# Kernel optimization log

Measured on AMD Instinct MI355X. Metric: run time of the kernel, lower is better.

The kernel has to match this reference:

```python
import jax, jax.numpy as jnp
import numpy as np

D = 1024
H = 16
HD = D // H

def setup_inputs() -> dict:
    key = jax.random.key(0)
    ks = jax.random.split(key, 6)
    tokens = jax.random.normal(ks[0], (2, 2048, D), dtype=jnp.float32)
    # LayerNorm params
    ln_gamma = jnp.ones((D,), dtype=jnp.float32)
    ln_beta = jnp.zeros((D,), dtype=jnp.float32)
    # qkv Linear (no bias): torch Linear weight is [3D, D]; store as [D, 3D] for x @ W
    w_qkv = jax.random.normal(ks[1], (D, 3 * D), dtype=jnp.float32) / np.sqrt(D)
    # output projection with bias
    w_proj = jax.random.normal(ks[2], (D, D), dtype=jnp.float32) / np.sqrt(D)
    b_proj = jax.random.normal(ks[3], (D,), dtype=jnp.float32) * 0.01
    return {"tokens": tokens, "ln_gamma": ln_gamma, "ln_beta": ln_beta,
            "w_qkv": w_qkv, "w_proj": w_proj, "b_proj": b_proj}

def reference(tokens, ln_gamma, ln_beta, w_qkv, w_proj, b_proj):
    B, S, _ = tokens.shape
    res = tokens
    # LayerNorm (eps=1e-5, torch default)
    mu = jnp.mean(tokens, axis=-1, keepdims=True)
    var = jnp.var(tokens, axis=-1, keepdims=True)
    x = (tokens - mu) * jax.lax.rsqrt(var + 1e-5) * ln_gamma + ln_beta
    # QKV projection -> [B, S, 3, H, HD] -> q,k,v each [B, H, S, HD]
    qkv = (x @ w_qkv).reshape(B, S, 3, H, HD)
    qkv = jnp.transpose(qkv, (2, 0, 3, 1, 4))
    q, k, v = qkv[0], qkv[1], qkv[2]
    scale = HD ** -0.5
    scores = jnp.einsum('bhsd,bhtd->bhst', q, k) * scale  # [B,H,S,S]
    attn = jax.nn.softmax(scores, axis=-1)
    dots = jnp.einsum('bhst,bhtd->bhsd', attn, v)          # [B,H,S,HD]
    dots = jnp.transpose(dots, (0, 2, 1, 3)).reshape(B, S, D)
    out = dots @ w_proj + b_proj
    return out + res
```

## Files before the change

### kernel.cpp

```cpp
#include <hip/hip_runtime.h>

typedef __bf16 bf16x8 __attribute__((ext_vector_type(8)));
typedef __bf16 bf16x4 __attribute__((ext_vector_type(4)));
typedef float f32x4 __attribute__((ext_vector_type(4)));
typedef unsigned short us8 __attribute__((ext_vector_type(8)));

__device__ __forceinline__ unsigned short f2bf(float f) {
  unsigned int u = __builtin_bit_cast(unsigned int, f);
  u += 0x7FFFu + ((u >> 16) & 1u);
  return (unsigned short)(u >> 16);
}
__device__ __forceinline__ float bf2f(unsigned short s) {
  return __builtin_bit_cast(float, (unsigned int)s << 16);
}

__device__ __forceinline__ void load_lds16(const void* g, void* l) {
  __builtin_amdgcn_global_load_lds(
      (const __attribute__((address_space(1))) unsigned int*)g,
      (__attribute__((address_space(3))) unsigned int*)l, 16, 0, 0);
}

#define MFMA16(a, b, c) __builtin_amdgcn_mfma_f32_16x16x32_bf16(a, b, c, 0, 0, 0)
#define EXP2(x) __builtin_amdgcn_exp2f(x)

constexpr int Dm = 1024, Ss = 2048;

__global__ __launch_bounds__(256) void prep_kernel(
    const float* __restrict__ x, const float* __restrict__ gamma,
    const float* __restrict__ beta, unsigned short* __restrict__ xbf,
    const float* __restrict__ wqkv, unsigned short* __restrict__ wqkvT,
    const float* __restrict__ wproj, unsigned short* __restrict__ wprojT) {
  __shared__ float tile[32][33];
  const int t = threadIdx.x;
  if (blockIdx.x < 4096) {
    const int row = blockIdx.x;
    const float4 v = reinterpret_cast<const float4*>(x + (size_t)row * Dm)[t];
    float s = v.x + v.y + v.z + v.w;
    float ss = v.x * v.x + v.y * v.y + v.z * v.z + v.w * v.w;
#pragma unroll
    for (int off = 1; off < 64; off <<= 1) {
      s += __shfl_xor(s, off);
      ss += __shfl_xor(ss, off);
    }
    float* sb = &tile[0][0];
    const int lane = t & 63, wid = t >> 6;
    if (lane == 0) { sb[wid] = s; sb[4 + wid] = ss; }
    __syncthreads();
    s = sb[0] + sb[1] + sb[2] + sb[3];
    ss = sb[4] + sb[5] + sb[6] + sb[7];
    const float mu = s * (1.0f / Dm);
    const float var = ss * (1.0f / Dm) - mu * mu;
    const float rs = rsqrtf(var + 1e-5f);
    const float4 g = reinterpret_cast<const float4*>(gamma)[t];
    const float4 bt = reinterpret_cast<const float4*>(beta)[t];
    ushort4 pack;
    pack.x = f2bf((v.x - mu) * rs * g.x + bt.x);
    pack.y = f2bf((v.y - mu) * rs * g.y + bt.y);
    pack.z = f2bf((v.z - mu) * rs * g.z + bt.z);
    pack.w = f2bf((v.w - mu) * rs * g.w + bt.w);
    reinterpret_cast<ushort4*>(xbf + (size_t)row * Dm)[t] = pack;
  } else {
    const float* in;
    unsigned short* out;
    int N, bxi, byi;
    const int id0 = blockIdx.x - 4096;
    if (id0 < 3072) {
      in = wqkv; out = wqkvT; N = 3072;
      bxi = id0 % 96; byi = id0 / 96;
    } else {
      in = wproj; out = wprojT; N = 1024;
      const int id = id0 - 3072;
      bxi = id % 32; byi = id / 32;
    }
    const int tx = t & 31, ty = t >> 5;
    const int n0 = bxi * 32, k0 = byi * 32;
#pragma unroll
    for (int i = 0; i < 4; i++)
      tile[ty + i * 8][tx] = in[(size_t)(k0 + ty + i * 8) * N + n0 + tx];
    __syncthreads();
#pragma unroll
    for (int i = 0; i < 4; i++)
      out[(size_t)(n0 + ty + i * 8) * 1024 + k0 + tx] = f2bf(tile[tx][ty + i * 8]);
  }
}

__global__ __launch_bounds__(512) void gemm256_kernel(
    const unsigned short* __restrict__ A, const unsigned short* __restrict__ Bt,
    unsigned short* __restrict__ Cbf, unsigned short* __restrict__ vt) {
  extern __shared__ char lds[];
  const int tid = threadIdx.x;
  const int lane = tid & 63, wid = tid >> 6;
  const int l15 = lane & 15, lg = lane >> 4;
  const int wr = wid >> 2, wc = wid & 3;
  const int lb = (blockIdx.x & 7) * 24 + (blockIdx.x >> 3);
  const int bx = lb % 12, by = lb / 12;
  const int bm = by * 256, bn = bx * 256;
  const int sswz = ((lane & 3) * 16) ^ (((lane >> 3) & 3) << 4);
  const char* Asrc = (const char*)A + (size_t)(bm + wid * 32 + (lane >> 2)) * 2048 + sswz;
  const char* Bsrc = (const char*)Bt + (size_t)(bn + wid * 32 + (lane >> 2)) * 2048 + sswz;
  const int rdsz = ((lg * 16) ^ (((l15 >> 1) & 3) << 4));

#define STG_A(kk_, bufT, tile_)                                                 \
  if ((tile_) < 16) {                                                           \
    _Pragma("unroll") for (int c = 0; c < 2; c++)                               \
      load_lds16(Asrc + (size_t)(c * 16) * 2048 + (tile_) * 128 + (kk_) * 64,   \
                 lds + ((bufT) * 2 + (kk_)) * 16384 + wid * 2048 + c * 1024);   \
  }
#define STG_B(kk_, bufT, tile_)                                                 \
  if ((tile_) < 16) {                                                           \
    _Pragma("unroll") for (int c = 0; c < 2; c++)                               \
      load_lds16(Bsrc + (size_t)(c * 16) * 2048 + (tile_) * 128 + (kk_) * 64,   \
                 lds + 65536 + ((bufT) * 2 + (kk_)) * 16384 + wid * 2048 +      \
                     c * 1024);                                                 \
  }
#define DS_A(buf_, kk_)                                                         \
  _Pragma("unroll") for (int mi = 0; mi < 8; mi++) {                            \
    const int r = wr * 128 + mi * 16 + l15;                                     \
    af[mi] = *(const bf16x8*)(lds + ((buf_) * 2 + (kk_)) * 16384 + r * 64 + rdsz); \
  }
#define DS_B(buf_, kk_, nh_)                                                    \
  _Pragma("unroll") for (int nj = 0; nj < 2; nj++) {                            \
    const int r = wc * 64 + (nh_) * 32 + nj * 16 + l15;                         \
    bfr[nj] = *(const bf16x8*)(lds + 65536 + ((buf_) * 2 + (kk_)) * 16384 +     \
                               r * 64 + rdsz);                                  \
  }
#define MM(nh_)                                                                 \
  __builtin_amdgcn_s_setprio(1);                                                \
  _Pragma("unroll") for (int mi = 0; mi < 8; mi++)                              \
      _Pragma("unroll") for (int nj = 0; nj < 2; nj++)                          \
          acc[mi][(nh_) * 2 + nj] = MFMA16(af[mi], bfr[nj], acc[mi][(nh_) * 2 + nj]); \
  __builtin_amdgcn_s_setprio(0);
#define GBAR __builtin_amdgcn_s_barrier()
#define LGKM0 asm volatile("s_waitcnt lgkmcnt(0)" ::: "memory")

  f32x4 acc[8][4] = {};

  STG_A(0, 0, 0); STG_B(0, 0, 0); STG_A(1, 0, 0); STG_B(1, 0, 0);
  STG_A(0, 1, 1); STG_B(0, 1, 1); STG_A(1, 1, 1);
  asm volatile("s_waitcnt vmcnt(6)" ::: "memory");
  GBAR;

  for (int i = 0; i < 8; ++i) {
    const int t2 = 2 * i + 2, t3 = 2 * i + 3;
    const bool last = (i == 7);
    bf16x8 af[8], bfr[2];
    DS_A(0, 0); DS_B(0, 0, 0); STG_B(1, 1, 2 * i + 1);
    GBAR; LGKM0; MM(0); GBAR;
    DS_B(0, 0, 1); STG_A(0, 0, t2);
    GBAR; LGKM0; MM(1); GBAR;
    DS_A(0, 1); DS_B(0, 1, 0); STG_B(0, 0, t2);
    GBAR; LGKM0; MM(0); GBAR;
    DS_B(0, 1, 1); STG_A(1, 0, t2);
    GBAR; LGKM0; MM(1);
    if (last) asm volatile("s_waitcnt vmcnt(0)" ::: "memory");
    else      asm volatile("s_waitcnt vmcnt(6)" ::: "memory");
    GBAR;
    DS_A(1, 0); DS_B(1, 0, 0); STG_B(1, 0, t2);
    GBAR; LGKM0; MM(0); GBAR;
    DS_B(1, 0, 1); STG_A(0, 1, t3);
    GBAR; LGKM0; MM(1); GBAR;
    DS_A(1, 1); DS_B(1, 1, 0); STG_B(0, 1, t3);
    GBAR; LGKM0; MM(0); GBAR;
    DS_B(1, 1, 1); STG_A(1, 1, t3);
    GBAR; LGKM0; MM(1);
    if (last) asm volatile("s_waitcnt vmcnt(0)" ::: "memory");
    else      asm volatile("s_waitcnt vmcnt(6)" ::: "memory");
    GBAR;
  }

#pragma unroll
  for (int mi = 0; mi < 8; mi++)
#pragma unroll
    for (int nj = 0; nj < 4; nj++) {
      const int m = bm + wr * 128 + mi * 16 + lg * 4;
      const int n = bn + wc * 64 + nj * 16 + l15;
      if (n < 2048) {
        const float sc = (n < 1024) ? 0.180336880f : 1.0f;
#pragma unroll
        for (int r = 0; r < 4; r++)
          Cbf[(size_t)(m + r) * 3072 + n] = f2bf(acc[mi][nj][r] * sc);
      } else {
        const int h = (n - 2048) >> 6, hd = (n - 2048) & 63;
        const int bq = m >> 11, s = m & 2047;
        bf16x4 o;
#pragma unroll
        for (int r = 0; r < 4; r++) o[r] = (__bf16)acc[mi][nj][r];
        *(bf16x4*)(vt + ((size_t)((bq << 4) + h) * 64 + hd) * 2048 + s) = o;
      }
    }
#undef STG_A
#undef STG_B
#undef DS_A
#undef DS_B
#undef MM
#undef GBAR
#undef LGKM0
}

template <int EPI, int BN>
__global__ __launch_bounds__(256) void gemm_kernel(
    const unsigned short* __restrict__ A, const unsigned short* __restrict__ Bt,
    int N, int K, int nbx, unsigned short* __restrict__ Cbf,
    unsigned short* __restrict__ vt, float* __restrict__ Cf,
    const float* __restrict__ bias, const float* __restrict__ resid) {
  __shared__ unsigned short Al[128 * 64];
  __shared__ unsigned short Bl[BN * 64];
  constexpr int NJ = BN / 32;
  const int tid = threadIdx.x;
  const int lane = tid & 63, wid = tid >> 6;
  const int l15 = lane & 15, lg = lane >> 4;
  const int wm = wid >> 1, wn = wid & 1;
  const int cpx = gridDim.x >> 3;
  const int lb = (blockIdx.x & 7) * cpx + (blockIdx.x >> 3);
  const int bx = lb % nbx, by = lb / nbx;
  const int bm = by * 128, bn = bx * BN;
  const int r8 = lane >> 3;
  const int swz = ((lane & 7) * 16) ^ (r8 << 4);
  const char* Ab = (const char*)A;
  const char* Bb = (const char*)Bt;
  f32x4 acc[4][NJ] = {};
  for (int k0 = 0; k0 < K; k0 += 64) {
    __syncthreads();
#pragma unroll
    for (int p = 0; p < 4; p++) {
      const int row = p * 32 + wid * 8 + r8;
      load_lds16(Ab + ((size_t)(bm + row) * K + k0) * 2 + swz,
                 (char*)Al + p * 4096 + wid * 1024);
    }
#pragma unroll
    for (int p = 0; p < BN / 32; p++) {
      const int row = p * 32 + wid * 8 + r8;
      load_lds16(Bb + ((size_t)(bn + row) * K + k0) * 2 + swz,
                 (char*)Bl + p * 4096 + wid * 1024);
    }
    __syncthreads();
#pragma unroll
    for (int kk = 0; kk < 2; kk++) {
      bf16x8 af[4], bfr[NJ];
#pragma unroll
      for (int mi = 0; mi < 4; mi++) {
        const int row = wm * 64 + mi * 16 + l15;
        af[mi] = *(const bf16x8*)((const char*)Al + row * 128 +
                                  ((kk * 64 + lg * 16) ^ ((row & 7) << 4)));
      }
#pragma unroll
      for (int nj = 0; nj < NJ; nj++) {
        const int row = wn * (BN / 2) + nj * 16 + l15;
        bfr[nj] = *(const bf16x8*)((const char*)Bl + row * 128 +
                                   ((kk * 64 + lg * 16) ^ ((row & 7) << 4)));
      }
#pragma unroll
      for (int mi = 0; mi < 4; mi++)
#pragma unroll
        for (int nj = 0; nj < NJ; nj++)
          acc[mi][nj] = MFMA16(af[mi], bfr[nj], acc[mi][nj]);
    }
  }
#pragma unroll
  for (int mi = 0; mi < 4; mi++)
#pragma unroll
    for (int nj = 0; nj < NJ; nj++) {
      const int m = bm + wm * 64 + mi * 16 + lg * 4;
      const int n = bn + wn * (BN / 2) + nj * 16 + l15;
      if (EPI == 0) {
        if (n < 2048) {
          const float sc = (n < 1024) ? 0.180336880f : 1.0f;
#pragma unroll
          for (int r = 0; r < 4; r++)
            Cbf[(size_t)(m + r) * N + n] = f2bf(acc[mi][nj][r] * sc);
        } else {
          const int h = (n - 2048) >> 6, hd = (n - 2048) & 63;
          const int bq = m >> 11, s = m & 2047;
          bf16x4 o;
#pragma unroll
          for (int r = 0; r < 4; r++) o[r] = (__bf16)acc[mi][nj][r];
          *(bf16x4*)(vt + ((size_t)((bq << 4) + h) * 64 + hd) * 2048 + s) = o;
        }
      } else {
#pragma unroll
        for (int r = 0; r < 4; r++) {
          const size_t idx = (size_t)(m + r) * N + n;
          Cf[idx] = acc[mi][nj][r] + bias[n] + resid[idx];
        }
      }
    }
}

__global__ __launch_bounds__(512) void attn_kernel(
    const unsigned short* __restrict__ qkv, const unsigned short* __restrict__ vt,
    unsigned short* part0, unsigned short* part1, float* __restrict__ ml) {
  __shared__ unsigned short Kb[2][64 * 64];
  __shared__ unsigned short Vb[2][64 * 64];
  __shared__ unsigned short Pl[8][32][64];
  const int tid = threadIdx.x, lane = tid & 63, wid = tid >> 6;
  const int l15 = lane & 15, lg = lane >> 4;
  const int lb = (blockIdx.x & 7) * 64 + (blockIdx.x >> 3);
  const int bh = lb >> 4, qt = (lb >> 1) & 7, half = lb & 1;
  const int b = bh >> 4, h = bh & 15;
  const int q0 = qt * 256 + wid * 32;
  const unsigned short* qbase = qkv + (size_t)(b * Ss) * 3072 + h * 64;
  const char* kbase = (const char*)(qkv + (size_t)(b * Ss) * 3072 + 1024 + h * 64);
  const char* vbase = (const char*)(vt + (size_t)bh * 64 * Ss);

  bf16x8 qf[2][2];
#pragma unroll
  for (int qj = 0; qj < 2; qj++)
#pragma unroll
    for (int kk = 0; kk < 2; kk++)
      qf[qj][kk] = *reinterpret_cast<const bf16x8*>(
          &qbase[(size_t)(q0 + qj * 16 + l15) * 3072 + kk * 32 + lg * 8]);

  f32x4 accT[4][2] = {};
  float psum[2] = {0.f, 0.f};

  const int srow = lane >> 3;
  const int swz = ((lane & 7) * 16) ^ (srow << 4);

#define STAGE(bufi, t0v)                                                          \
  {                                                                               \
    load_lds16(kbase + (size_t)((t0v) + wid * 8 + srow) * 6144 + swz,             \
               (char*)&Kb[bufi][0] + wid * 1024);                                 \
    load_lds16(vbase + (size_t)(wid * 8 + srow) * 4096 + (size_t)(t0v) * 2 + swz, \
               (char*)&Vb[bufi][0] + wid * 1024);                                 \
  }

  const int t0base = half * 1024;
  STAGE(0, t0base);

  for (int itr = 0; itr < 16; itr++) {
    const int cur = itr & 1;
    asm volatile("s_waitcnt vmcnt(0)" ::: "memory");
    __builtin_amdgcn_s_barrier();
    if (itr + 1 < 16) STAGE(cur ^ 1, t0base + (itr + 1) * 64);

    const char* kcur = (const char*)&Kb[cur][0];
    const char* vcur = (const char*)&Vb[cur][0];

    f32x4 accs[4][2] = {};
    __builtin_amdgcn_s_setprio(1);
#pragma unroll
    for (int kk = 0; kk < 2; kk++) {
      bf16x8 kf[4];
#pragma unroll
      for (int kvi = 0; kvi < 4; kvi++) {
        const int rk = kvi * 16 + l15;
        kf[kvi] = *(const bf16x8*)(kcur + rk * 128 +
                                   ((kk * 64 + lg * 16) ^ ((rk & 7) << 4)));
      }
#pragma unroll
      for (int kvi = 0; kvi < 4; kvi++)
#pragma unroll
        for (int qj = 0; qj < 2; qj++)
          accs[kvi][qj] = MFMA16(kf[kvi], qf[qj][kk], accs[kvi][qj]);
    }
    __builtin_amdgcn_s_setprio(0);

#pragma unroll
    for (int qj = 0; qj < 2; qj++) {
      const int prow = qj * 16 + l15;
      char* prl = (char*)&Pl[wid][prow][0];
      float ps = 0.f;
#pragma unroll
      for (int kvi = 0; kvi < 4; kvi++) {
        bf16x4 pk;
#pragma unroll
        for (int r = 0; r < 4; r++) {
          const float p = EXP2(accs[kvi][qj][r]);
          ps += p;
          pk[r] = (__bf16)p;
        }
        *(bf16x4*)(prl + ((kvi * 32 + lg * 8) ^ ((l15 & 7) << 4))) = pk;
      }
      psum[qj] += ps;
    }

    asm volatile("s_waitcnt lgkmcnt(0)" ::: "memory");
    __builtin_amdgcn_sched_barrier(0);

    __builtin_amdgcn_s_setprio(1);
#pragma unroll
    for (int kk2 = 0; kk2 < 2; kk2++) {
      bf16x8 pf[2], vf[4];
#pragma unroll
      for (int qj = 0; qj < 2; qj++)
        pf[qj] = *(const bf16x8*)((const char*)&Pl[wid][qj * 16 + l15][0] +
                                  ((kk2 * 64 + lg * 16) ^ ((l15 & 7) << 4)));
#pragma unroll
      for (int nj = 0; nj < 4; nj++) {
        const int rv = nj * 16 + l15;
        vf[nj] = *(const bf16x8*)(vcur + rv * 128 +
                                  ((kk2 * 64 + lg * 16) ^ ((rv & 7) << 4)));
      }
#pragma unroll
      for (int nj = 0; nj < 4; nj++)
#pragma unroll
        for (int qj = 0; qj < 2; qj++)
          accT[nj][qj] = MFMA16(vf[nj], pf[qj], accT[nj][qj]);
    }
    __builtin_amdgcn_s_setprio(0);
  }

#pragma unroll
  for (int qj = 0; qj < 2; qj++) {
    psum[qj] += __shfl_xor(psum[qj], 16);
    psum[qj] += __shfl_xor(psum[qj], 32);
  }
  unsigned short* pout = half ? part1 : part0;
#pragma unroll
  for (int qj = 0; qj < 2; qj++) {
    const float rl = 1.0f / psum[qj];
    const int q = q0 + qj * 16 + l15;
#pragma unroll
    for (int nj = 0; nj < 4; nj++) {
      bf16x4 o;
#pragma unroll
      for (int r = 0; r < 4; r++) o[r] = (__bf16)(accT[nj][qj][r] * rl);
      *(bf16x4*)(pout + (size_t)(b * Ss + q) * Dm + h * 64 + nj * 16 + lg * 4) = o;
    }
  }
  if (lg == 0) {
#pragma unroll
    for (int qj = 0; qj < 2; qj++)
      ml[half * 65536 + bh * 2048 + q0 + qj * 16 + l15] = psum[qj];
  }
}

__global__ __launch_bounds__(256) void combine_kernel(
    const unsigned short* p0, const unsigned short* __restrict__ p1,
    const float* __restrict__ ml, unsigned short* dots) {
  const int t = blockIdx.x * 256 + threadIdx.x;
  const int hd8 = t & 7;
  const int h = (t >> 3) & 15;
  const int row = t >> 7;
  const int b = row >> 11, s = row & 2047;
  const int bh = b * 16 + h;
  const float w0 = ml[bh * 2048 + s];
  const float w1 = ml[65536 + bh * 2048 + s];
  const float inv = 1.0f / (w0 + w1);
  const size_t off = (size_t)row * 1024 + h * 64 + hd8 * 8;
  const us8 a = *(const us8*)(p0 + off);
  const us8 c = *(const us8*)(p1 + off);
  us8 o;
#pragma unroll
  for (int j = 0; j < 8; j++)
    o[j] = f2bf((bf2f(a[j]) * w0 + bf2f(c[j]) * w1) * inv);
  *(us8*)(dots + off) = o;
}

extern "C" void kernel_launch(void* const* d_in, const int* in_sizes, int n_in,
                              void* d_out, int out_size, void* d_ws, size_t ws_size,
                              hipStream_t stream) {
  const float* tokens = (const float*)d_in[0];
  const float* ln_g = (const float*)d_in[1];
  const float* ln_b = (const float*)d_in[2];
  const float* w_qkv = (const float*)d_in[3];
  const float* w_proj = (const float*)d_in[4];
  const float* b_proj = (const float*)d_in[5];
  float* out = (float*)d_out;

  char* ws = (char*)d_ws;
  unsigned short* x_bf = (unsigned short*)(ws);
  unsigned short* wqkvT = (unsigned short*)(ws + 8388608);
  unsigned short* wprojT = (unsigned short*)(ws + 14680064);
  unsigned short* qkvraw = (unsigned short*)(ws + 16777216);
  unsigned short* vt = (unsigned short*)(ws + 41943040);
  unsigned short* part1 = (unsigned short*)(ws + 50331648);
  float* ml = (float*)(ws + 58720256);
  unsigned short* dots = x_bf;

  hipFuncSetAttribute((const void*)gemm256_kernel,
                      hipFuncAttributeMaxDynamicSharedMemorySize, 131072);

  prep_kernel<<<8192, 256, 0, stream>>>(tokens, ln_g, ln_b, x_bf,
                                        w_qkv, wqkvT, w_proj, wprojT);
  gemm256_kernel<<<192, 512, 131072, stream>>>(x_bf, wqkvT, qkvraw, vt);
  attn_kernel<<<512, 512, 0, stream>>>(qkvraw, vt, dots, part1, ml);
  combine_kernel<<<2048, 256, 0, stream>>>(dots, part1, ml, dots);
  gemm_kernel<1, 64><<<512, 256, 0, stream>>>(
      dots, wprojT, 1024, 1024, 16, nullptr, nullptr, out, b_proj, tokens);
}
```

Measured before the change: 115.8 us.

## Fuse split-KV combine into attention kernel via last-block atomic flag

Removes the separate combine kernel launch. Each pair of attention blocks that handle the two KV halves of the same query tile increments an atomic counter after a threadfence, and the second block to finish merges both partial outputs into dots using the stored softmax sums. Partial buffers move to dedicated workspace regions, and a memset clears the flags on each call. This saves a launch and a pass over the partials, but adds a serialized tail of combine work in the finishing blocks plus a memset launch.

New measurement: 237.2 us. 2.05x slower.

```diff
diff --git a/kernel.cpp b/kernel.cpp
--- a/kernel.cpp
+++ b/kernel.cpp
@@ -288,10 +288,12 @@
 
 __global__ __launch_bounds__(512) void attn_kernel(
     const unsigned short* __restrict__ qkv, const unsigned short* __restrict__ vt,
-    unsigned short* part0, unsigned short* part1, float* __restrict__ ml) {
+    unsigned short* part0, unsigned short* part1, float* __restrict__ ml,
+    unsigned short* __restrict__ dots, int* __restrict__ flags) {
   __shared__ unsigned short Kb[2][64 * 64];
   __shared__ unsigned short Vb[2][64 * 64];
   __shared__ unsigned short Pl[8][32][64];
+  __shared__ int loser_sh;
   const int tid = threadIdx.x, lane = tid & 63, wid = tid >> 6;
   const int l15 = lane & 15, lg = lane >> 4;
   const int lb = (blockIdx.x & 7) * 64 + (blockIdx.x >> 3);
@@ -423,28 +425,29 @@
     for (int qj = 0; qj < 2; qj++)
       ml[half * 65536 + bh * 2048 + q0 + qj * 16 + l15] = psum[qj];
   }
-}
-
-__global__ __launch_bounds__(256) void combine_kernel(
-    const unsigned short* p0, const unsigned short* __restrict__ p1,
-    const float* __restrict__ ml, unsigned short* dots) {
-  const int t = blockIdx.x * 256 + threadIdx.x;
-  const int hd8 = t & 7;
-  const int h = (t >> 3) & 15;
-  const int row = t >> 7;
-  const int b = row >> 11, s = row & 2047;
-  const int bh = b * 16 + h;
-  const float w0 = ml[bh * 2048 + s];
-  const float w1 = ml[65536 + bh * 2048 + s];
-  const float inv = 1.0f / (w0 + w1);
-  const size_t off = (size_t)row * 1024 + h * 64 + hd8 * 8;
-  const us8 a = *(const us8*)(p0 + off);
-  const us8 c = *(const us8*)(p1 + off);
-  us8 o;
-#pragma unroll
-  for (int j = 0; j < 8; j++)
-    o[j] = f2bf((bf2f(a[j]) * w0 + bf2f(c[j]) * w1) * inv);
-  *(us8*)(dots + off) = o;
+
+  __threadfence();
+  __syncthreads();
+  if (tid == 0) loser_sh = atomicAdd(&flags[lb >> 1], 1);
+  __syncthreads();
+  if (loser_sh == 1) {
+    const int q0b = qt * 256;
+    for (int c = tid; c < 2048; c += 512) {
+      const int row = c >> 3, col8 = c & 7;
+      const int q = q0b + row;
+      const float w0 = ml[bh * 2048 + q];
+      const float w1 = ml[65536 + bh * 2048 + q];
+      const float inv = 1.0f / (w0 + w1);
+      const size_t off = (size_t)(b * Ss + q) * Dm + h * 64 + col8 * 8;
+      const us8 a = *(const us8*)(part0 + off);
+      const us8 cc = *(const us8*)(part1 + off);
+      us8 o;
+#pragma unroll
+      for (int j = 0; j < 8; j++)
+        o[j] = f2bf((bf2f(a[j]) * w0 + bf2f(cc[j]) * w1) * inv);
+      *(us8*)(dots + off) = o;
+    }
+  }
 }
 
 extern "C" void kernel_launch(void* const* d_in, const int* in_sizes, int n_in,
@@ -464,18 +467,20 @@
   unsigned short* wprojT = (unsigned short*)(ws + 14680064);
   unsigned short* qkvraw = (unsigned short*)(ws + 16777216);
   unsigned short* vt = (unsigned short*)(ws + 41943040);
-  unsigned short* part1 = (unsigned short*)(ws + 50331648);
-  float* ml = (float*)(ws + 58720256);
+  unsigned short* part0 = (unsigned short*)(ws + 50331648);
+  unsigned short* part1 = (unsigned short*)(ws + 58720256);
+  float* ml = (float*)(ws + 67108864);
+  int* flags = (int*)(ws + 68157440);
   unsigned short* dots = x_bf;
 
   hipFuncSetAttribute((const void*)gemm256_kernel,
                       hipFuncAttributeMaxDynamicSharedMemorySize, 131072);
 
+  hipMemsetAsync(flags, 0, 1024, stream);
   prep_kernel<<<8192, 256, 0, stream>>>(tokens, ln_g, ln_b, x_bf,
                                         w_qkv, wqkvT, w_proj, wprojT);
   gemm256_kernel<<<192, 512, 131072, stream>>>(x_bf, wqkvT, qkvraw, vt);
-  attn_kernel<<<512, 512, 0, stream>>>(qkvraw, vt, dots, part1, ml);
-  combine_kernel<<<2048, 256, 0, stream>>>(dots, part1, ml, dots);
+  attn_kernel<<<512, 512, 0, stream>>>(qkvraw, vt, part0, part1, ml, dots, flags);
   gemm_kernel<1, 64><<<512, 256, 0, stream>>>(
       dots, wprojT, 1024, 1024, 16, nullptr, nullptr, out, b_proj, tokens);
 }
```
